# Kernel tuning notes

Measured on AMD Instinct MI355X. Metric: run time of the kernel, lower is better.

Reference implementation:

```python
import math
import jax, jax.numpy as jnp
import numpy as np

B, S, E = 4, 2048, 768
H, D = 12, 64
LOCAL_H, GLOBAL_H = 8, 4
WINDOW_BASE, MIN_W, MAX_W = 128, 32, 512
GLOBAL_RATIO = 0.1
MASK_VALUE = -1e9


def setup_inputs() -> dict:
    key = jax.random.key(0)
    k1, k2, k3 = jax.random.split(key, 3)
    return {
        "x": jax.random.normal(k1, (B, S, E), dtype=jnp.float32),
        "w_attn": jax.random.normal(k2, (E, 3 * E), dtype=jnp.float32) * 0.02,
        "b_attn": jnp.zeros((3 * E,), dtype=jnp.float32),
        "w_proj": jax.random.normal(k3, (E, E), dtype=jnp.float32) * 0.02,
        "b_proj": jnp.zeros((E,), dtype=jnp.float32),
    }


def _masks(seq_len: int):
    # dynamic window (adaptive): base * sqrt(S/base), clamped
    w = int(WINDOW_BASE * math.sqrt(seq_len / WINDOW_BASE))
    w = max(MIN_W, min(w, MAX_W))
    half = w // 2
    i = jnp.arange(seq_len)[:, None]
    j = jnp.arange(seq_len)[None, :]
    # local: window band then causal override -> allowed iff i-half <= j <= i
    local_allowed = (j >= i - half) & (j <= i)
    local_mask = jnp.where(local_allowed, 0.0, MASK_VALUE).astype(jnp.float32)
    # global: columns at linspace positions allowed for all rows, plus full causal
    n_glob = max(1, int(seq_len * GLOBAL_RATIO))
    gpos = jnp.linspace(0.0, seq_len - 1, n_glob).astype(jnp.int32)
    is_gcol = jnp.zeros((seq_len,), dtype=bool).at[gpos].set(True)
    global_allowed = (j <= i) | is_gcol[None, :]
    global_mask = jnp.where(global_allowed, 0.0, MASK_VALUE).astype(jnp.float32)
    return local_mask, global_mask


def _attend(q, k, v, mask):
    # q,k,v: [B,h,S,D]; mask: [S,S]
    scale = 1.0 / math.sqrt(q.shape[-1])
    scores = jnp.einsum("bhqd,bhkd->bhqk", q, k) * scale + mask[None, None]
    w = jax.nn.softmax(scores, axis=-1)
    return jnp.einsum("bhqk,bhkd->bhqd", w, v)


def reference(x, w_attn, b_attn, w_proj, b_proj):
    b, s, _ = x.shape
    qkv = x @ w_attn + b_attn                       # [B,S,3E]
    q, k, v = jnp.split(qkv, 3, axis=-1)
    def heads(t):
        return t.reshape(b, s, H, D).transpose(0, 2, 1, 3)  # [B,H,S,D]
    q, k, v = heads(q), heads(k), heads(v)
    local_mask, global_mask = _masks(s)
    local_out = _attend(q[:, :LOCAL_H], k[:, :LOCAL_H], v[:, :LOCAL_H], local_mask)
    global_out = _attend(q[:, LOCAL_H:], k[:, LOCAL_H:], v[:, LOCAL_H:], global_mask)
    attn = jnp.concatenate([local_out, global_out], axis=1)  # heads 0..7 local, 8..11 global
    attn = attn.transpose(0, 2, 1, 3).reshape(b, s, E)
    return attn @ w_proj + b_proj
```

## Files before the change

kernel.cpp:

```cpp
#include <hip/hip_runtime.h>
#include <stdint.h>


#define NH 12
#define SQ 2048

typedef __bf16 bf16x8 __attribute__((ext_vector_type(8)));
typedef float f32x4 __attribute__((ext_vector_type(4)));

#define GLOAD_LDS16(g, l)                                                      \
  __builtin_amdgcn_global_load_lds(                                            \
      (__attribute__((address_space(1))) void*)(g),                            \
      (__attribute__((address_space(3))) void*)(l), 16, 0, 0)

__device__ __forceinline__ unsigned short bfbits(float f) {
  __bf16 h = (__bf16)f;
  return *(unsigned short*)&h;
}

__global__ __launch_bounds__(256) void prep(
    const float* __restrict__ x, unsigned short* __restrict__ xb,
    const float* __restrict__ w_attn, unsigned short* __restrict__ wattnT,
    const float* __restrict__ w_proj, unsigned short* __restrict__ wprojT) {
  const int bid = blockIdx.x, t = threadIdx.x;
  if (bid < 512) {
    const int n4 = 8192 * 768 / 4;
    for (int i = bid * 256 + t; i < n4; i += 512 * 256) {
      float4 v = ((const float4*)x)[i];
      ((ushort4*)xb)[i] = make_ushort4(bfbits(v.x), bfbits(v.y), bfbits(v.z), bfbits(v.w));
    }
    return;
  }
  __shared__ float tile[32][33];
  const float* in; unsigned short* out; int K, N, tl;
  if (bid < 512 + 72 * 24) { in = w_attn; out = wattnT; K = 768; N = 2304; tl = bid - 512; }
  else                     { in = w_proj; out = wprojT; K = 768; N = 768;  tl = bid - 512 - 72 * 24; }
  const int tpr = N / 32;
  const int n0 = (tl % tpr) * 32, k0 = (tl / tpr) * 32;
  const int tx = t & 31, ty = t >> 5;
  for (int r = ty; r < 32; r += 8) tile[r][tx] = in[(size_t)(k0 + r) * N + n0 + tx];
  __syncthreads();
  for (int r = ty; r < 32; r += 8) out[(size_t)(n0 + r) * K + k0 + tx] = bfbits(tile[tx][r]);
}

__global__ __launch_bounds__(256) void vprep(const unsigned short* __restrict__ QKV,
                                             unsigned short* __restrict__ Vtb,
                                             unsigned short* __restrict__ Kg,
                                             unsigned short* __restrict__ VgT,
                                             int* __restrict__ gidx) {
  const int id = blockIdx.x, t = threadIdx.x;
  if (id < 1536) {
    const int bh = id >> 5, b = bh / NH, h = bh % NH;
    const int s0 = (id & 31) * 64;
    __shared__ unsigned short T[64][72];
    const int r = t >> 2, c0 = (t & 3) * 16;
    const size_t src = (size_t)(b * SQ + s0 + r) * 2304 + 1536 + h * 64 + c0;
    *(uint4*)&T[r][c0]     = *(const uint4*)&QKV[src];
    *(uint4*)&T[r][c0 + 8] = *(const uint4*)&QKV[src + 8];
    __syncthreads();
    unsigned short pk[16];
#pragma unroll
    for (int z = 0; z < 16; ++z) pk[z] = T[c0 + z][r];
    size_t dst = (size_t)bh * 131072 + (size_t)r * 2048 + s0 + c0;
    *(uint4*)&Vtb[dst]     = *(uint4*)&pk[0];
    *(uint4*)&Vtb[dst + 8] = *(uint4*)&pk[8];
    return;
  }
  const int g = id - 1536;
  const int bh = g >> 3, y = g & 7;
  const int b = bh >> 2, h = 8 + (bh & 3);
  if (g == 0) {
    int c = t;
    gidx[c] = (c < 203) ? (int)((double)c * (2047.0 / 203.0)) : ((c == 203) ? 2047 : -1);
  }
  {
    int c = t, ch = y;
    int col = (c < 203) ? (int)((double)c * (2047.0 / 203.0)) : ((c == 203) ? 2047 : -1);
    uint4 v = {0u, 0u, 0u, 0u};
    if (col >= 0) v = *(const uint4*)&QKV[(size_t)(b * SQ + col) * 2304 + 768 + h * 64 + ch * 8];
    *(uint4*)&Kg[((size_t)bh * 256 + c) * 64 + ch * 8] = v;
  }
  {
    int d = t >> 2;
    int cb = (t & 3) * 64 + y * 8;
    for (int cc = 0; cc < 8; ++cc) {
      int c = cb + cc;
      int col = (c < 203) ? (int)((double)c * (2047.0 / 203.0)) : ((c == 203) ? 2047 : -1);
      unsigned short v = 0;
      if (col >= 0) v = QKV[(size_t)(b * SQ + col) * 2304 + 1536 + h * 64 + d];
      VgT[((size_t)bh * 64 + d) * 256 + c] = v;
    }
  }
}

__device__ __forceinline__ void gemm_mainloop(
    const unsigned short* __restrict__ A, const unsigned short* __restrict__ BT,
    int m0, int n0, int tid,
    unsigned short* As, unsigned short* Bs,
    f32x4 acc[4][4]) {
  const int lane = tid & 63, wave = tid >> 6;
  const int wm = wave >> 1, wn = wave & 1;
  const int ln = lane & 15, quad = lane >> 4;
  const int arow = wave * 16 + (lane >> 2);
  const int acol = (lane & 3) * 8;

#pragma unroll
  for (int mi = 0; mi < 4; ++mi)
#pragma unroll
    for (int ni = 0; ni < 4; ++ni) acc[mi][ni] = (f32x4){0.f, 0.f, 0.f, 0.f};

  for (int kt = 0; kt < 12; ++kt) {
    const int k0 = kt * 64;
    __syncthreads();
#pragma unroll
    for (int p = 0; p < 2; ++p) {
      const int ldso = (p * 64 + wave * 16) * 32;
      GLOAD_LDS16(A  + (size_t)(m0 + p * 64 + arow) * 768 + k0 + acol,       &As[ldso]);
      GLOAD_LDS16(A  + (size_t)(m0 + p * 64 + arow) * 768 + k0 + 32 + acol,  &As[4096 + ldso]);
      GLOAD_LDS16(BT + (size_t)(n0 + p * 64 + arow) * 768 + k0 + acol,       &Bs[ldso]);
      GLOAD_LDS16(BT + (size_t)(n0 + p * 64 + arow) * 768 + k0 + 32 + acol,  &Bs[4096 + ldso]);
    }
    __syncthreads();
#pragma unroll
    for (int kh = 0; kh < 2; ++kh) {
      const int base = kh * 4096;
      bf16x8 aF[4], bF[4];
#pragma unroll
      for (int mi = 0; mi < 4; ++mi)
        aF[mi] = *(const bf16x8*)&As[base + (wm * 64 + mi * 16 + ln) * 32 + quad * 8];
#pragma unroll
      for (int ni = 0; ni < 4; ++ni)
        bF[ni] = *(const bf16x8*)&Bs[base + (wn * 64 + ni * 16 + ln) * 32 + quad * 8];
#pragma unroll
      for (int mi = 0; mi < 4; ++mi)
#pragma unroll
        for (int ni = 0; ni < 4; ++ni)
          acc[mi][ni] = __builtin_amdgcn_mfma_f32_16x16x32_bf16(aF[mi], bF[ni], acc[mi][ni], 0, 0, 0);
    }
  }
}

__global__ __launch_bounds__(256) void qkv_gemm(
    const unsigned short* __restrict__ Xb, const unsigned short* __restrict__ WT,
    const float* __restrict__ bias, unsigned short* __restrict__ Out) {
  __shared__ __attribute__((aligned(16))) unsigned short As[2 * 128 * 32];
  __shared__ __attribute__((aligned(16))) unsigned short Bs[2 * 128 * 32];
  f32x4 acc[4][4];
  const int m0 = blockIdx.y * 128, n0 = blockIdx.x * 128;
  const int tid = threadIdx.x;
  gemm_mainloop(Xb, WT, m0, n0, tid, As, Bs, acc);
  const int lane = tid & 63, wave = tid >> 6;
  const int wm = wave >> 1, wn = wave & 1, ln = lane & 15, quad = lane >> 4;
#pragma unroll
  for (int mi = 0; mi < 4; ++mi)
#pragma unroll
    for (int ni = 0; ni < 4; ++ni) {
      int n = n0 + wn * 64 + ni * 16 + ln;
      float bs = bias[n];
#pragma unroll
      for (int rg = 0; rg < 4; ++rg) {
        int m = m0 + wm * 64 + mi * 16 + quad * 4 + rg;
        Out[(size_t)m * 2304 + n] = bfbits(acc[mi][ni][rg] + bs);
      }
    }
}

__global__ __launch_bounds__(256) void proj_gemm(
    const unsigned short* __restrict__ Ab, const unsigned short* __restrict__ WT,
    const float* __restrict__ bias, float* __restrict__ Out) {
  __shared__ __attribute__((aligned(16))) unsigned short As[2 * 128 * 32];
  __shared__ __attribute__((aligned(16))) unsigned short Bs[2 * 128 * 32];
  f32x4 acc[4][4];
  const int m0 = blockIdx.y * 128, n0 = blockIdx.x * 128;
  const int tid = threadIdx.x;
  gemm_mainloop(Ab, WT, m0, n0, tid, As, Bs, acc);
  const int lane = tid & 63, wave = tid >> 6;
  const int wm = wave >> 1, wn = wave & 1, ln = lane & 15, quad = lane >> 4;
#pragma unroll
  for (int mi = 0; mi < 4; ++mi)
#pragma unroll
    for (int ni = 0; ni < 4; ++ni)
#pragma unroll
      for (int rg = 0; rg < 4; ++rg) {
        int m = m0 + wm * 64 + mi * 16 + quad * 4 + rg;
        int n = n0 + wn * 64 + ni * 16 + ln;
        Out[(size_t)m * 768 + n] = acc[mi][ni][rg] + bias[n];
      }
}

__global__ __launch_bounds__(256, 6) void attn_kernel(
    const unsigned short* __restrict__ QKV,
    const unsigned short* __restrict__ Vtb,
    const unsigned short* __restrict__ Kg, const unsigned short* __restrict__ VgT,
    const int* __restrict__ gidx,
    unsigned short* __restrict__ AOut,
    unsigned short* __restrict__ Opart,
    float* __restrict__ Lpart) {
  __shared__ __attribute__((aligned(16))) unsigned short Ks[64 * 72];
  __shared__ __attribute__((aligned(16))) unsigned short Vs[64 * 72];

  const int gid = blockIdx.x;
  int b, h, qb, kb_begin, kb_end, slot = 0;
  bool do_g = false, multi = false;
  if (gid < 1184) {
    int bh = gid / 74, rem = gid % 74;
    b = bh >> 2; h = 8 + (bh & 3);
    int part;
    if (rem < 9)       { qb = rem; part = 0; }
    else if (rem < 27) { int z = rem - 9;  qb = 9 + (z >> 1);  part = z & 1; }
    else if (rem < 54) { int z = rem - 27; int q3 = z / 3; qb = 18 + q3; part = z - 3 * q3; }
    else               { int z = rem - 54; qb = 27 + (z >> 2); part = z & 3; }
    kb_begin = part * 9;
    kb_end = min(part * 9 + 8, qb);
    do_g = (part == 0);
    multi = (qb >= 9);
    slot = (bh * 32 + qb) * 4 + part;
  } else {
    int lid = gid - 1184;
    int bh = lid >> 5; b = bh >> 3; h = bh & 7; qb = lid & 31;
    kb_begin = (qb > 4) ? qb - 4 : 0; kb_end = qb;
  }
  const int qb0 = qb * 64;
  const bool is_local = (h < 8);
  const int tid = threadIdx.x, lane = tid & 63, wave = tid >> 6;
  const int ln = lane & 15, quad = lane >> 4;
  const int bh48 = b * NH + h;
  const int bhg = (b << 2) | (h & 3);

  const size_t qoff = (size_t)(b * SQ + qb0 + wave * 16 + ln) * 2304 + h * 64;
  bf16x8 qA0 = *(const bf16x8*)&QKV[qoff + quad * 8];
  bf16x8 qA1 = *(const bf16x8*)&QKV[qoff + 32 + quad * 8];

  bf16x8 onesF;
#pragma unroll
  for (int z = 0; z < 8; ++z) onesF[z] = (__bf16)1.0f;

  f32x4 o[4];
  f32x4 ls = (f32x4){0.f, 0.f, 0.f, 0.f};
#pragma unroll
  for (int dt = 0; dt < 4; ++dt) o[dt] = (f32x4){0.f, 0.f, 0.f, 0.f};

  const int nc = kb_end - kb_begin + 1;
  const int ntiles = nc + (do_g ? 4 : 0);
  const int irow = qb0 + wave * 16 + quad * 4;
  const int iw = qb0 + wave * 16;
  const int sr = tid >> 3, sch = tid & 7;

  for (int t = 0; t < ntiles; ++t) {
    const bool gph = (t >= nc);
    const int kstart = gph ? 0 : (kb_begin + t) * 64;
    const int kg0 = gph ? (t - nc) * 64 : 0;
    __syncthreads();
    if (!gph) {
#pragma unroll
      for (int p = 0; p < 2; ++p) {
        int row = p * 32 + sr;
        *(uint4*)&Ks[row * 72 + sch * 8] =
            *(const uint4*)&QKV[(size_t)(b * SQ + kstart + row) * 2304 + 768 + h * 64 + sch * 8];
        *(uint4*)&Vs[row * 72 + sch * 8] =
            *(const uint4*)&Vtb[(size_t)bh48 * 131072 + (size_t)row * 2048 + kstart + sch * 8];
      }
    } else {
#pragma unroll
      for (int p = 0; p < 2; ++p) {
        int row = p * 32 + sr;
        *(uint4*)&Ks[row * 72 + sch * 8] =
            *(const uint4*)&Kg[((size_t)bhg * 256 + kg0 + row) * 64 + sch * 8];
        *(uint4*)&Vs[row * 72 + sch * 8] =
            *(const uint4*)&VgT[((size_t)bhg * 64 + row) * 256 + kg0 + sch * 8];
      }
    }
    __syncthreads();

    float sc[4][4];
    const bool full = !gph && (kstart + 63 <= iw) && (!is_local || kstart >= iw - 241);
#pragma unroll
    for (int nt = 0; nt < 4; ++nt) {
      bf16x8 kF0 = *(const bf16x8*)&Ks[(nt * 16 + ln) * 72 + quad * 8];
      bf16x8 kF1 = *(const bf16x8*)&Ks[(nt * 16 + ln) * 72 + 32 + quad * 8];
      f32x4 c = (f32x4){0.f, 0.f, 0.f, 0.f};
      c = __builtin_amdgcn_mfma_f32_16x16x32_bf16(qA0, kF0, c, 0, 0, 0);
      c = __builtin_amdgcn_mfma_f32_16x16x32_bf16(qA1, kF1, c, 0, 0, 0);
      if (full) {
#pragma unroll
        for (int rg = 0; rg < 4; ++rg) sc[nt][rg] = c[rg] * 0.125f - 8.f;
      } else if (!gph) {
        int j = kstart + nt * 16 + ln;
#pragma unroll
        for (int rg = 0; rg < 4; ++rg) {
          int i = irow + rg;
          bool ok = is_local ? (j >= i - 256 && j <= i) : (j <= i);
          sc[nt][rg] = ok ? (c[rg] * 0.125f - 8.f) : -1e9f;
        }
      } else {
        int jg = gidx[kg0 + nt * 16 + ln];
#pragma unroll
        for (int rg = 0; rg < 4; ++rg) {
          bool ok = jg > (irow + rg);
          sc[nt][rg] = ok ? (c[rg] * 0.125f - 8.f) : -1e9f;
        }
      }
    }
    __syncthreads();

    __bf16* P = (__bf16*)Ks;
#pragma unroll
    for (int rg = 0; rg < 4; ++rg) {
      int prow = (wave * 16 + quad * 4 + rg) * 72;
#pragma unroll
      for (int nt = 0; nt < 4; ++nt)
        P[prow + nt * 16 + ln] = (__bf16)__expf(sc[nt][rg]);
    }
    bf16x8 pF0 = *(const bf16x8*)&Ks[(wave * 16 + ln) * 72 + quad * 8];
    bf16x8 pF1 = *(const bf16x8*)&Ks[(wave * 16 + ln) * 72 + 32 + quad * 8];
    ls = __builtin_amdgcn_mfma_f32_16x16x32_bf16(pF0, onesF, ls, 0, 0, 0);
    ls = __builtin_amdgcn_mfma_f32_16x16x32_bf16(pF1, onesF, ls, 0, 0, 0);
#pragma unroll
    for (int dt = 0; dt < 4; ++dt) {
      bf16x8 vF0 = *(const bf16x8*)&Vs[(dt * 16 + ln) * 72 + quad * 8];
      bf16x8 vF1 = *(const bf16x8*)&Vs[(dt * 16 + ln) * 72 + 32 + quad * 8];
      o[dt] = __builtin_amdgcn_mfma_f32_16x16x32_bf16(pF0, vF0, o[dt], 0, 0, 0);
      o[dt] = __builtin_amdgcn_mfma_f32_16x16x32_bf16(pF1, vF1, o[dt], 0, 0, 0);
    }
  }

  if (gid >= 1184 || !multi) {
#pragma unroll
    for (int dt = 0; dt < 4; ++dt)
#pragma unroll
      for (int rg = 0; rg < 4; ++rg) {
        int row = b * SQ + qb0 + wave * 16 + quad * 4 + rg;
        int e = h * 64 + dt * 16 + ln;
        AOut[(size_t)row * 768 + e] = bfbits(o[dt][rg] / ls[rg]);
      }
  } else {
#pragma unroll
    for (int dt = 0; dt < 4; ++dt)
#pragma unroll
      for (int rg = 0; rg < 4; ++rg) {
        int row = wave * 16 + quad * 4 + rg;
        Opart[(size_t)slot * 4096 + row * 64 + dt * 16 + ln] = bfbits(o[dt][rg]);
      }
    if (ln == 0) {
#pragma unroll
      for (int rg = 0; rg < 4; ++rg)
        Lpart[(size_t)slot * 64 + wave * 16 + quad * 4 + rg] = ls[rg];
    }
  }
}

__global__ __launch_bounds__(256) void combine_parts(
    const unsigned short* __restrict__ Opart, const float* __restrict__ Lpart,
    unsigned short* __restrict__ AOut) {
  const int bid = blockIdx.x;
  const int bh = bid / 23, qb = bid % 23 + 9;
  const int b = bh >> 2, h = 8 + (bh & 3);
  const int np = qb / 9 + 1;
  const int t = threadIdx.x, r = t >> 2, c0 = (t & 3) * 16;
  const int slot0 = (bh * 32 + qb) * 4;
  float acc[16];
#pragma unroll
  for (int z = 0; z < 16; ++z) acc[z] = 0.f;
  float l = 0.f;
  for (int p = 0; p < np; ++p) {
    const unsigned short* src = &Opart[(size_t)(slot0 + p) * 4096 + r * 64 + c0];
    bf16x8 v0 = *(const bf16x8*)&src[0];
    bf16x8 v1 = *(const bf16x8*)&src[8];
#pragma unroll
    for (int z = 0; z < 8; ++z) { acc[z] += (float)v0[z]; acc[8 + z] += (float)v1[z]; }
    l += Lpart[(size_t)(slot0 + p) * 64 + r];
  }
  float inv = 1.f / l;
  unsigned short pk[16];
#pragma unroll
  for (int z = 0; z < 16; ++z) pk[z] = bfbits(acc[z] * inv);
  size_t dst = (size_t)(b * SQ + qb * 64 + r) * 768 + h * 64 + c0;
  *(uint4*)&AOut[dst]     = *(uint4*)&pk[0];
  *(uint4*)&AOut[dst + 8] = *(uint4*)&pk[8];
}

extern "C" void kernel_launch(void* const* d_in, const int* in_sizes, int n_in,
                              void* d_out, int out_size, void* d_ws, size_t ws_size,
                              hipStream_t stream) {
  const float* x      = (const float*)d_in[0];
  const float* w_attn = (const float*)d_in[1];
  const float* b_attn = (const float*)d_in[2];
  const float* w_proj = (const float*)d_in[3];
  const float* b_proj = (const float*)d_in[4];
  float* out = (float*)d_out;

  char* ws = (char*)d_ws;
  size_t off = 0;
  auto alloc = [&](size_t bytes) {
    void* p = ws + off;
    off += (bytes + 255) & ~(size_t)255;
    return p;
  };
  unsigned short* xb     = (unsigned short*)alloc((size_t)8192 * 768 * 2);
  unsigned short* wattnT = (unsigned short*)alloc((size_t)2304 * 768 * 2);
  unsigned short* wprojT = (unsigned short*)alloc((size_t)768 * 768 * 2);
  unsigned short* qkvb   = (unsigned short*)alloc((size_t)8192 * 2304 * 2);
  unsigned short* Vtb    = (unsigned short*)alloc((size_t)48 * 64 * 2048 * 2);
  unsigned short* Kgb    = (unsigned short*)alloc((size_t)16 * 256 * 64 * 2);
  unsigned short* VgTb   = (unsigned short*)alloc((size_t)16 * 64 * 256 * 2);
  int* gidxb             = (int*)alloc((size_t)256 * 4);
  unsigned short* Opartb = (unsigned short*)alloc((size_t)2048 * 4096 * 2);
  float* Lpartb          = (float*)alloc((size_t)2048 * 64 * 4);
  unsigned short* attnb  = xb;

  prep<<<dim3(512 + 72 * 24 + 24 * 24), dim3(256), 0, stream>>>(
      x, xb, w_attn, wattnT, w_proj, wprojT);
  qkv_gemm<<<dim3(18, 64), dim3(256), 0, stream>>>(xb, wattnT, b_attn, qkvb);
  vprep<<<dim3(1536 + 128), dim3(256), 0, stream>>>(qkvb, Vtb, Kgb, VgTb, gidxb);
  attn_kernel<<<dim3(2208), dim3(256), 0, stream>>>(qkvb, Vtb, Kgb, VgTb, gidxb,
                                                    attnb, Opartb, Lpartb);
  combine_parts<<<dim3(368), dim3(256), 0, stream>>>(Opartb, Lpartb, attnb);
  proj_gemm<<<dim3(6, 64), dim3(256), 0, stream>>>(attnb, wprojT, b_proj, out);
}
```

Before: 210.7 us.

## Prefetch next K/V tile into registers, add separate P buffer, rebalance global split

The attention loop now loads the next K/V tile into registers while the current tile is being computed, and writes P to a dedicated shared buffer so one barrier per iteration can be dropped. The global-head work is re-split into a unified virtual-tile space covering global columns plus causal blocks, with up to five parts per query block, so blocks do more even amounts of work. Combine slot indexing is updated to match. The cost is more registers and shared memory per block, with launch bounds lowered from 6 to 5 waves, which may reduce occupancy.

```diff
diff --git a/kernel.cpp b/kernel.cpp
--- a/kernel.cpp
+++ b/kernel.cpp
@@ -188,7 +188,7 @@
       }
 }
 
-__global__ __launch_bounds__(256, 6) void attn_kernel(
+__global__ __launch_bounds__(256, 5) void attn_kernel(
     const unsigned short* __restrict__ QKV,
     const unsigned short* __restrict__ Vtb,
     const unsigned short* __restrict__ Kg, const unsigned short* __restrict__ VgT,
@@ -198,27 +198,28 @@
     float* __restrict__ Lpart) {
   __shared__ __attribute__((aligned(16))) unsigned short Ks[64 * 72];
   __shared__ __attribute__((aligned(16))) unsigned short Vs[64 * 72];
+  __shared__ __attribute__((aligned(16))) unsigned short Ps[64 * 72];
 
   const int gid = blockIdx.x;
-  int b, h, qb, kb_begin, kb_end, slot = 0;
-  bool do_g = false, multi = false;
-  if (gid < 1184) {
-    int bh = gid / 74, rem = gid % 74;
+  int b, h, qb, vt0, vt1;
+  bool multi = false;
+  if (gid < 1536) {
+    int bh = gid / 96, rem = gid % 96;
     b = bh >> 2; h = 8 + (bh & 3);
     int part;
-    if (rem < 9)       { qb = rem; part = 0; }
-    else if (rem < 27) { int z = rem - 9;  qb = 9 + (z >> 1);  part = z & 1; }
-    else if (rem < 54) { int z = rem - 27; int q3 = z / 3; qb = 18 + q3; part = z - 3 * q3; }
-    else               { int z = rem - 54; qb = 27 + (z >> 2); part = z & 3; }
-    kb_begin = part * 9;
-    kb_end = min(part * 9 + 8, qb);
-    do_g = (part == 0);
-    multi = (qb >= 9);
-    slot = (bh * 32 + qb) * 4 + part;
+    if (rem < 4)       { qb = rem;                               part = 0; }
+    else if (rem < 20) { int z = rem - 4;  qb = 4 + (z >> 1);    part = z & 1; }
+    else if (rem < 44) { int z = rem - 20; int q = z / 3; qb = 12 + q; part = z - 3 * q; }
+    else if (rem < 76) { int z = rem - 44; qb = 20 + (z >> 2);   part = z & 3; }
+    else               { int z = rem - 76; int q = z / 5; qb = 28 + q; part = z - 5 * q; }
+    vt0 = part * 8;
+    vt1 = min(vt0 + 8, qb + 5);
+    multi = (qb >= 4);
   } else {
-    int lid = gid - 1184;
+    int lid = gid - 1536;
     int bh = lid >> 5; b = bh >> 3; h = bh & 7; qb = lid & 31;
-    kb_begin = (qb > 4) ? qb - 4 : 0; kb_end = qb;
+    vt0 = ((qb > 4) ? qb - 4 : 0) + 4;
+    vt1 = qb + 5;
   }
   const int qb0 = qb * 64;
   const bool is_local = (h < 8);
@@ -240,38 +241,42 @@
 #pragma unroll
   for (int dt = 0; dt < 4; ++dt) o[dt] = (f32x4){0.f, 0.f, 0.f, 0.f};
 
-  const int nc = kb_end - kb_begin + 1;
-  const int ntiles = nc + (do_g ? 4 : 0);
   const int irow = qb0 + wave * 16 + quad * 4;
   const int iw = qb0 + wave * 16;
   const int sr = tid >> 3, sch = tid & 7;
 
-  for (int t = 0; t < ntiles; ++t) {
-    const bool gph = (t >= nc);
-    const int kstart = gph ? 0 : (kb_begin + t) * 64;
-    const int kg0 = gph ? (t - nc) * 64 : 0;
+  uint4 pk0, pk1, pv0, pv1;
+  auto issue_load = [&](int vt) {
+    if (vt >= 4) {
+      const int kstart = (vt - 4) * 64;
+      const size_t ko = (size_t)(b * SQ + kstart + sr) * 2304 + 768 + h * 64 + sch * 8;
+      pk0 = *(const uint4*)&QKV[ko];
+      pk1 = *(const uint4*)&QKV[ko + (size_t)32 * 2304];
+      const size_t vo = (size_t)bh48 * 131072 + (size_t)sr * 2048 + kstart + sch * 8;
+      pv0 = *(const uint4*)&Vtb[vo];
+      pv1 = *(const uint4*)&Vtb[vo + 32 * 2048];
+    } else {
+      const int kg0 = vt * 64;
+      pk0 = *(const uint4*)&Kg[((size_t)bhg * 256 + kg0 + sr) * 64 + sch * 8];
+      pk1 = *(const uint4*)&Kg[((size_t)bhg * 256 + kg0 + 32 + sr) * 64 + sch * 8];
+      pv0 = *(const uint4*)&VgT[((size_t)bhg * 64 + sr) * 256 + kg0 + sch * 8];
+      pv1 = *(const uint4*)&VgT[((size_t)bhg * 64 + 32 + sr) * 256 + kg0 + sch * 8];
+    }
+  };
+  issue_load(vt0);
+
+  for (int vt = vt0; vt < vt1; ++vt) {
+    const bool gph = (vt < 4);
     __syncthreads();
-    if (!gph) {
-#pragma unroll
-      for (int p = 0; p < 2; ++p) {
-        int row = p * 32 + sr;
-        *(uint4*)&Ks[row * 72 + sch * 8] =
-            *(const uint4*)&QKV[(size_t)(b * SQ + kstart + row) * 2304 + 768 + h * 64 + sch * 8];
-        *(uint4*)&Vs[row * 72 + sch * 8] =
-            *(const uint4*)&Vtb[(size_t)bh48 * 131072 + (size_t)row * 2048 + kstart + sch * 8];
-      }
-    } else {
-#pragma unroll
-      for (int p = 0; p < 2; ++p) {
-        int row = p * 32 + sr;
-        *(uint4*)&Ks[row * 72 + sch * 8] =
-            *(const uint4*)&Kg[((size_t)bhg * 256 + kg0 + row) * 64 + sch * 8];
-        *(uint4*)&Vs[row * 72 + sch * 8] =
-            *(const uint4*)&VgT[((size_t)bhg * 64 + row) * 256 + kg0 + sch * 8];
-      }
-    }
+    *(uint4*)&Ks[sr * 72 + sch * 8]        = pk0;
+    *(uint4*)&Ks[(32 + sr) * 72 + sch * 8] = pk1;
+    *(uint4*)&Vs[sr * 72 + sch * 8]        = pv0;
+    *(uint4*)&Vs[(32 + sr) * 72 + sch * 8] = pv1;
     __syncthreads();
-
+    if (vt + 1 < vt1) issue_load(vt + 1);
+
+    const int kstart = (vt - 4) * 64;
+    const int kg0 = vt * 64;
     float sc[4][4];
     const bool full = !gph && (kstart + 63 <= iw) && (!is_local || kstart >= iw - 241);
 #pragma unroll
@@ -301,9 +306,8 @@
         }
       }
     }
-    __syncthreads();
-
-    __bf16* P = (__bf16*)Ks;
+
+    __bf16* P = (__bf16*)Ps;
 #pragma unroll
     for (int rg = 0; rg < 4; ++rg) {
       int prow = (wave * 16 + quad * 4 + rg) * 72;
@@ -311,8 +315,8 @@
       for (int nt = 0; nt < 4; ++nt)
         P[prow + nt * 16 + ln] = (__bf16)__expf(sc[nt][rg]);
     }
-    bf16x8 pF0 = *(const bf16x8*)&Ks[(wave * 16 + ln) * 72 + quad * 8];
-    bf16x8 pF1 = *(const bf16x8*)&Ks[(wave * 16 + ln) * 72 + 32 + quad * 8];
+    bf16x8 pF0 = *(const bf16x8*)&Ps[(wave * 16 + ln) * 72 + quad * 8];
+    bf16x8 pF1 = *(const bf16x8*)&Ps[(wave * 16 + ln) * 72 + 32 + quad * 8];
     ls = __builtin_amdgcn_mfma_f32_16x16x32_bf16(pF0, onesF, ls, 0, 0, 0);
     ls = __builtin_amdgcn_mfma_f32_16x16x32_bf16(pF1, onesF, ls, 0, 0, 0);
 #pragma unroll
@@ -324,7 +328,7 @@
     }
   }
 
-  if (gid >= 1184 || !multi) {
+  if (gid >= 1536 || !multi) {
 #pragma unroll
     for (int dt = 0; dt < 4; ++dt)
 #pragma unroll
@@ -339,12 +343,12 @@
 #pragma unroll
       for (int rg = 0; rg < 4; ++rg) {
         int row = wave * 16 + quad * 4 + rg;
-        Opart[(size_t)slot * 4096 + row * 64 + dt * 16 + ln] = bfbits(o[dt][rg]);
+        Opart[(size_t)gid * 4096 + row * 64 + dt * 16 + ln] = bfbits(o[dt][rg]);
       }
     if (ln == 0) {
 #pragma unroll
       for (int rg = 0; rg < 4; ++rg)
-        Lpart[(size_t)slot * 64 + wave * 16 + quad * 4 + rg] = ls[rg];
+        Lpart[(size_t)gid * 64 + wave * 16 + quad * 4 + rg] = ls[rg];
     }
   }
 }
@@ -353,11 +357,15 @@
     const unsigned short* __restrict__ Opart, const float* __restrict__ Lpart,
     unsigned short* __restrict__ AOut) {
   const int bid = blockIdx.x;
-  const int bh = bid / 23, qb = bid % 23 + 9;
+  const int bh = bid / 28, qb = bid % 28 + 4;
   const int b = bh >> 2, h = 8 + (bh & 3);
-  const int np = qb / 9 + 1;
+  int C, np;
+  if (qb < 12)      { C = 2 * qb - 4;  np = 2; }
+  else if (qb < 20) { C = 3 * qb - 16; np = 3; }
+  else if (qb < 28) { C = 4 * qb - 36; np = 4; }
+  else              { C = 5 * qb - 64; np = 5; }
+  const int slot0 = bh * 96 + C;
   const int t = threadIdx.x, r = t >> 2, c0 = (t & 3) * 16;
-  const int slot0 = (bh * 32 + qb) * 4;
   float acc[16];
 #pragma unroll
   for (int z = 0; z < 16; ++z) acc[z] = 0.f;
@@ -404,16 +412,16 @@
   unsigned short* Kgb    = (unsigned short*)alloc((size_t)16 * 256 * 64 * 2);
   unsigned short* VgTb   = (unsigned short*)alloc((size_t)16 * 64 * 256 * 2);
   int* gidxb             = (int*)alloc((size_t)256 * 4);
-  unsigned short* Opartb = (unsigned short*)alloc((size_t)2048 * 4096 * 2);
-  float* Lpartb          = (float*)alloc((size_t)2048 * 64 * 4);
+  unsigned short* Opartb = (unsigned short*)alloc((size_t)1536 * 4096 * 2);
+  float* Lpartb          = (float*)alloc((size_t)1536 * 64 * 4);
   unsigned short* attnb  = xb;
 
   prep<<<dim3(512 + 72 * 24 + 24 * 24), dim3(256), 0, stream>>>(
       x, xb, w_attn, wattnT, w_proj, wprojT);
   qkv_gemm<<<dim3(18, 64), dim3(256), 0, stream>>>(xb, wattnT, b_attn, qkvb);
   vprep<<<dim3(1536 + 128), dim3(256), 0, stream>>>(qkvb, Vtb, Kgb, VgTb, gidxb);
-  attn_kernel<<<dim3(2208), dim3(256), 0, stream>>>(qkvb, Vtb, Kgb, VgTb, gidxb,
+  attn_kernel<<<dim3(2560), dim3(256), 0, stream>>>(qkvb, Vtb, Kgb, VgTb, gidxb,
                                                     attnb, Opartb, Lpartb);
-  combine_parts<<<dim3(368), dim3(256), 0, stream>>>(Opartb, Lpartb, attnb);
+  combine_parts<<<dim3(448), dim3(256), 0, stream>>>(Opartb, Lpartb, attnb);
   proj_gemm<<<dim3(6, 64), dim3(256), 0, stream>>>(attnb, wprojT, b_proj, out);
 }
```

Measured after the change: 211.6 us. Within noise of the previous version (+0.4%).
